# Kernel optimization log

Measured on AMD Instinct MI355X. Metric: run time of the kernel, lower is better.

Reference implementation:

```python
import jax, jax.numpy as jnp
import numpy as np

B, T, C = 2, 2048, 2048
H = 16
HD = C // H  # 128; kv_size == hidden_size so kv head dim == HD


def setup_inputs() -> dict:
    key = jax.random.key(0)
    ks = jax.random.split(key, 5)
    s = 0.02
    return {
        "x": jax.random.normal(ks[0], (B, T, C), dtype=jnp.float32),
        "Wq": jax.random.normal(ks[1], (C, C), dtype=jnp.float32) * s,
        "Wk": jax.random.normal(ks[2], (C, C), dtype=jnp.float32) * s,
        "Wv": jax.random.normal(ks[3], (C, C), dtype=jnp.float32) * s,
        "Wo": jax.random.normal(ks[4], (C, C), dtype=jnp.float32) * s,
    }


def reference(x, Wq, Wk, Wv, Wo):
    # Linear(bias=False): y = x @ W.T
    q = (x @ Wq.T).reshape(B, T, H, HD).transpose(0, 2, 1, 3)  # [B,H,T,HD]
    k = (x @ Wk.T).reshape(B, T, H, HD).transpose(0, 2, 1, 3)
    v = (x @ Wv.T).reshape(B, T, H, HD).transpose(0, 2, 1, 3)
    scale = 1.0 / np.sqrt(HD).astype(np.float32)
    att = jnp.einsum("bhqd,bhkd->bhqk", q, k) * scale  # [B,H,T,T]
    att = jax.nn.softmax(att, axis=-1)
    y = jnp.einsum("bhqk,bhkd->bhqd", att, v)  # [B,H,T,HD]
    y = y.transpose(0, 2, 1, 3).reshape(B, T, C)
    return y @ Wo.T
```

## Files before the change

kernel.cpp:

```cpp
#include <hip/hip_runtime.h>
#include <hip/hip_bf16.h>

typedef __attribute__((ext_vector_type(8))) short short8;
typedef __attribute__((ext_vector_type(4))) float f32x4;
typedef __attribute__((ext_vector_type(16))) float f32x16;
typedef unsigned short u16;
typedef unsigned int u32;

__device__ __forceinline__ u16 f2bf(float f){
  __hip_bfloat16 h = __float2bfloat16(f);
  return *reinterpret_cast<u16*>(&h);
}

__device__ __forceinline__ void gld16(const void* g, void* l){
  __builtin_amdgcn_global_load_lds((const __attribute__((address_space(1))) void*)g,
                                   (__attribute__((address_space(3))) void*)l, 16, 0, 0);
}

#define SCHED0() __builtin_amdgcn_sched_barrier(0)

__global__ __launch_bounds__(256) void cvt_kernel(const float* __restrict__ src,
                                                  u16* __restrict__ dst, int n){
  int i0 = (blockIdx.x*256 + threadIdx.x)*4;
  int stride = gridDim.x*256*4;
  for (int i = i0; i < n; i += stride){
    float4 f = *reinterpret_cast<const float4*>(src + i);
    ushort4 u;
    u.x = f2bf(f.x); u.y = f2bf(f.y); u.z = f2bf(f.z); u.w = f2bf(f.w);
    *reinterpret_cast<ushort4*>(dst + i) = u;
  }
}

__device__ __forceinline__ void gemm256_body(const u16* __restrict__ A,
    const u16* __restrict__ W, void* __restrict__ outp, float scale, int epi)
{
  __shared__ alignas(16) u16 Lds[2*24576];
  const int tid = threadIdx.x;
  const int w = tid>>6, l = tid&63;
  const int l15 = l&15, lg = l>>4;
  const int wm = w>>1, wn = w&1;
  const int row0 = blockIdx.y*256, col0 = blockIdx.x*128;
  constexpr int K = 2048;
  constexpr int NT = K/64;

  f32x4 acc[4][4];
  #pragma unroll
  for (int i=0;i<4;i++)
    #pragma unroll
    for (int j=0;j<4;j++)
      #pragma unroll
      for (int r=0;r<4;r++) acc[i][j][r] = 0.f;

  int arow[2], acol[2], brow[2], bcol[2];
  #pragma unroll
  for (int p=0;p<2;p++){
    int s = p*512 + tid;
    arow[p] = s>>2;  acol[p] = ((s&3) ^ (arow[p]&3))*8;
    brow[p] = s>>3;  bcol[p] = ((s&7) ^ (brow[p]&7))*8;
  }

  auto stageB = [&](int buf, int kt){
    #pragma unroll
    for (int p=0;p<2;p++)
      gld16(W + (size_t)(col0 + brow[p])*K + kt*64 + bcol[p],
            &Lds[buf*24576 + 16384 + (p*512 + w*64)*8]);
  };
  auto stageA = [&](int buf, int kt, int kh){
    #pragma unroll
    for (int p=0;p<2;p++)
      gld16(A + (size_t)(row0 + arow[p])*K + kt*64 + kh*32 + acol[p],
            &Lds[buf*24576 + kh*8192 + (p*512 + w*64)*8]);
  };
  auto readA = [&](int buf, int ks, short8* af){
    #pragma unroll
    for (int i=0;i<4;i++){
      int r = wm*64 + i*16 + l15;
      int byt = buf*49152 + ks*16384 + r*64 + ((lg ^ (r&3))<<4);
      af[i] = *reinterpret_cast<const short8*>((const char*)Lds + byt);
    }
  };
  auto readB = [&](int buf, int ks, short8* bf){
    #pragma unroll
    for (int j=0;j<4;j++){
      int r = wn*64 + j*16 + l15;
      int byt = buf*49152 + 32768 + r*128 + ((((ks<<2)|lg) ^ (r&7))<<4);
      bf[j] = *reinterpret_cast<const short8*>((const char*)Lds + byt);
    }
  };

  stageB(0, 0); stageA(0, 0, 0); stageA(0, 0, 1);
  SCHED0();
  asm volatile("s_waitcnt vmcnt(2)" ::: "memory");
  __builtin_amdgcn_s_barrier();
  SCHED0();

  int cur = 0;
  for (int t=0; t<NT; ++t){
    int nxt = (t+1) & (NT-1);
    int nbuf = cur^1;
    short8 af[4], bf[4];
    stageB(nbuf, nxt);
    stageA(nbuf, nxt, 0);
    readA(cur, 0, af); readB(cur, 0, bf);
    asm volatile("s_waitcnt lgkmcnt(0)" ::: "memory");
    SCHED0();
    __builtin_amdgcn_s_setprio(1);
    #pragma unroll
    for (int i=0;i<4;i++)
      #pragma unroll
      for (int j=0;j<4;j++)
        acc[i][j] = __builtin_amdgcn_mfma_f32_16x16x32_bf16(af[i], bf[j], acc[i][j], 0, 0, 0);
    __builtin_amdgcn_s_setprio(0);
    SCHED0();
    asm volatile("s_waitcnt vmcnt(4)" ::: "memory");
    __builtin_amdgcn_s_barrier();
    SCHED0();
    stageA(nbuf, nxt, 1);
    readA(cur, 1, af); readB(cur, 1, bf);
    asm volatile("s_waitcnt lgkmcnt(0)" ::: "memory");
    SCHED0();
    __builtin_amdgcn_s_setprio(1);
    #pragma unroll
    for (int i=0;i<4;i++)
      #pragma unroll
      for (int j=0;j<4;j++)
        acc[i][j] = __builtin_amdgcn_mfma_f32_16x16x32_bf16(af[i], bf[j], acc[i][j], 0, 0, 0);
    __builtin_amdgcn_s_setprio(0);
    SCHED0();
    asm volatile("s_waitcnt vmcnt(2)" ::: "memory");
    __builtin_amdgcn_s_barrier();
    SCHED0();
    cur ^= 1;
  }

  if (epi == 0){
    u16* O = (u16*)outp;
    #pragma unroll
    for (int i=0;i<4;i++)
      #pragma unroll
      for (int j=0;j<4;j++)
        #pragma unroll
        for (int r=0;r<4;r++){
          int m = row0 + wm*64 + i*16 + lg*4 + r;
          int n = col0 + wn*64 + j*16 + l15;
          int b = m >> 11, tt = m & 2047;
          int h = n >> 7,  d = n & 127;
          O[(((size_t)(b*16 + h)*2048 + tt)<<7) + d] = f2bf(acc[i][j][r] * scale);
        }
  } else if (epi == 2){
    u16* O = (u16*)outp;
    #pragma unroll
    for (int i=0;i<4;i++)
      #pragma unroll
      for (int j=0;j<4;j++){
        int m0 = row0 + wm*64 + i*16 + lg*4;
        int n  = col0 + wn*64 + j*16 + l15;
        int b = m0 >> 11, tt = m0 & 2047;
        int h = n >> 7,  d = n & 127;
        ushort4 u;
        u.x = f2bf(acc[i][j][0]); u.y = f2bf(acc[i][j][1]);
        u.z = f2bf(acc[i][j][2]); u.w = f2bf(acc[i][j][3]);
        *reinterpret_cast<ushort4*>(&O[(((size_t)(b*16 + h)<<7) + d)*2048 + tt]) = u;
      }
  } else {
    float* O = (float*)outp;
    #pragma unroll
    for (int i=0;i<4;i++)
      #pragma unroll
      for (int j=0;j<4;j++)
        #pragma unroll
        for (int r=0;r<4;r++){
          int m = row0 + wm*64 + i*16 + lg*4 + r;
          int n = col0 + wn*64 + j*16 + l15;
          O[(size_t)m*2048 + n] = acc[i][j][r];
        }
  }
}

__global__ __launch_bounds__(512,2) void gemm_qkv(const u16* __restrict__ A,
    const u16* __restrict__ Wq, const u16* __restrict__ Wk, const u16* __restrict__ Wv,
    u16* __restrict__ qo, u16* __restrict__ ko, u16* __restrict__ vt, float qscale)
{
  const u16* W; void* O; float sc; int epi;
  if (blockIdx.z == 0){ W = Wq; O = qo; sc = qscale; epi = 0; }
  else if (blockIdx.z == 1){ W = Wk; O = ko; sc = 1.f; epi = 0; }
  else { W = Wv; O = vt; sc = 1.f; epi = 2; }
  gemm256_body(A, W, O, sc, epi);
}

__global__ __launch_bounds__(512,2) void gemm_out(const u16* __restrict__ A,
    const u16* __restrict__ W, float* __restrict__ O)
{
  gemm256_body(A, W, O, 1.f, 1);
}

__global__ __launch_bounds__(256,2) void attn_kernel(
    const u16* __restrict__ Q, const u16* __restrict__ Kg,
    const u16* __restrict__ Vt, u16* __restrict__ Y)
{
  __shared__ alignas(16) u16 Ks[2][64*128];
  __shared__ alignas(16) u16 Vs[2][64*128];
  const int tid = threadIdx.x;
  const int w = tid>>6, l = tid&63;
  const int l31 = l&31, hi = l>>5;
  const int bh_swz = ((blockIdx.x&7)*64 + (blockIdx.x>>3));
  const int bh = bh_swz >> 4;
  const int q0 = (bh_swz & 15) * 128;

  short8 qf[8];
  #pragma unroll
  for (int ds=0; ds<8; ds++)
    qf[ds] = *reinterpret_cast<const short8*>(
        Q + ((size_t)bh*2048 + q0 + w*32 + l31)*128 + ds*16 + hi*8);

  f32x16 accO[4];
  #pragma unroll
  for (int dt=0;dt<4;dt++)
    #pragma unroll
    for (int r=0;r<16;r++) accO[dt][r] = 0.f;
  float mrun = -1e30f, lrun = 0.f;

  int krow_[4], kcol_[4], vd_[4], vkv_[4];
  #pragma unroll
  for (int p=0;p<4;p++){
    int s = p*256 + tid;
    int r = s>>4, c = s&15;
    int cu = c ^ (r&15);
    krow_[p] = r;  kcol_[p] = cu*8;
    vd_[p] = r*2 + (cu>>3);  vkv_[p] = (cu&7)*8;
  }

  auto stage = [&](int buf, int kvt){
    int kv0 = kvt*64;
    #pragma unroll
    for (int p=0;p<4;p++)
      gld16(Kg + ((size_t)bh*2048 + kv0 + krow_[p])*128 + kcol_[p],
            &Ks[buf][(size_t)(p*256 + w*64)*8]);
    #pragma unroll
    for (int p=0;p<4;p++)
      gld16(Vt + ((size_t)bh*128 + vd_[p])*2048 + kv0 + vkv_[p],
            &Vs[buf][(size_t)(p*256 + w*64)*8]);
  };

  stage(0, 0);
  __syncthreads();

  int cur = 0;
  for (int kvt=0; kvt<32; ++kvt){
    if (kvt+1 < 32) stage(cur^1, kvt+1);

    f32x16 accS[2];
    #pragma unroll
    for (int kt=0;kt<2;kt++)
      #pragma unroll
      for (int r=0;r<16;r++) accS[kt][r] = 0.f;
    #pragma unroll
    for (int kt=0;kt<2;kt++){
      #pragma unroll
      for (int ds=0;ds<8;ds++){
        int row = kt*32 + l31;
        int byt = row*256 + (((ds*2 + hi) ^ (row&15))<<4);
        short8 kf = *reinterpret_cast<const short8*>((const char*)(&Ks[cur][0]) + byt);
        accS[kt] = __builtin_amdgcn_mfma_f32_32x32x16_bf16(kf, qf[ds], accS[kt], 0, 0, 0);
      }
    }

    float pmax = accS[0][0];
    #pragma unroll
    for (int kt=0;kt<2;kt++)
      #pragma unroll
      for (int r=0;r<16;r++) pmax = fmaxf(pmax, accS[kt][r]);
    pmax = fmaxf(pmax, __shfl_xor(pmax, 32, 64));
    if (__any(pmax > mrun + 8.f)){
      float mn = fmaxf(mrun, pmax);
      float c = __expf(mrun - mn);
      mrun = mn;
      lrun *= c;
      #pragma unroll
      for (int r=0;r<16;r++){
        int qrow = (r&3) + 8*(r>>2) + 4*hi;
        float cr = __shfl(c, qrow, 64);
        #pragma unroll
        for (int dt=0;dt<4;dt++) accO[dt][r] *= cr;
      }
    }

    float rs = 0.f;
    short8 pa[4];
    #pragma unroll
    for (int kt=0;kt<2;kt++){
      #pragma unroll
      for (int b=0;b<2;b++){
        float e0 = __expf(accS[kt][b*8+0] - mrun);
        float e1 = __expf(accS[kt][b*8+1] - mrun);
        float e2 = __expf(accS[kt][b*8+2] - mrun);
        float e3 = __expf(accS[kt][b*8+3] - mrun);
        float e4 = __expf(accS[kt][b*8+4] - mrun);
        float e5 = __expf(accS[kt][b*8+5] - mrun);
        float e6 = __expf(accS[kt][b*8+6] - mrun);
        float e7 = __expf(accS[kt][b*8+7] - mrun);
        rs += (e0+e1)+(e2+e3)+(e4+e5)+(e6+e7);
        u32 x01 = (u32)f2bf(e0) | ((u32)f2bf(e1)<<16);
        u32 x23 = (u32)f2bf(e2) | ((u32)f2bf(e3)<<16);
        u32 y01 = (u32)f2bf(e4) | ((u32)f2bf(e5)<<16);
        u32 y23 = (u32)f2bf(e6) | ((u32)f2bf(e7)<<16);
        u32 sx_x01 = __shfl_xor(x01, 32, 64);
        u32 sx_x23 = __shfl_xor(x23, 32, 64);
        u32 sx_y01 = __shfl_xor(y01, 32, 64);
        u32 sx_y23 = __shfl_xor(y23, 32, 64);
        int4 wv;
        wv.x = (int)(hi ? sx_y01 : x01);
        wv.y = (int)(hi ? sx_y23 : x23);
        wv.z = (int)(hi ? y01 : sx_x01);
        wv.w = (int)(hi ? y23 : sx_x23);
        pa[kt*2+b] = *reinterpret_cast<short8*>(&wv);
      }
    }
    rs += __shfl_xor(rs, 32, 64);
    lrun += rs;

    #pragma unroll
    for (int dt=0;dt<4;dt++){
      #pragma unroll
      for (int ks=0;ks<4;ks++){
        int d = dt*32 + l31;
        int cu = (d&1)*8 + ks*2 + hi;
        int byt = (d>>1)*256 + ((cu ^ ((d>>1)&15))<<4);
        short8 vf = *reinterpret_cast<const short8*>((const char*)(&Vs[cur][0]) + byt);
        accO[dt] = __builtin_amdgcn_mfma_f32_32x32x16_bf16(pa[ks], vf, accO[dt], 0, 0, 0);
      }
    }

    __syncthreads();
    cur ^= 1;
  }

  const int b_ = bh >> 4, h_ = bh & 15;
  float inv = 1.f / lrun;
  #pragma unroll
  for (int r=0;r<16;r++){
    int qrow = (r&3) + 8*(r>>2) + 4*hi;
    float lr = __shfl(inv, qrow, 64);
    int t = q0 + w*32 + qrow;
    #pragma unroll
    for (int dt=0;dt<4;dt++){
      int d = dt*32 + l31;
      Y[((size_t)b_*2048 + t)*2048 + h_*128 + d] = f2bf(accO[dt][r] * lr);
    }
  }
}

extern "C" void kernel_launch(void* const* d_in, const int* in_sizes, int n_in,
                              void* d_out, int out_size, void* d_ws, size_t ws_size,
                              hipStream_t stream)
{
  const float* x  = (const float*)d_in[0];
  const float* Wq = (const float*)d_in[1];
  const float* Wk = (const float*)d_in[2];
  const float* Wv = (const float*)d_in[3];
  const float* Wo = (const float*)d_in[4];
  float* out = (float*)d_out;
  char* ws = (char*)d_ws;

  const size_t MB = 1024*1024;
  u16* xb  = (u16*)(ws);
  u16* wqb = (u16*)(ws + 16*MB);
  u16* wkb = (u16*)(ws + 24*MB);
  u16* wvb = (u16*)(ws + 32*MB);
  u16* wob = (u16*)(ws + 40*MB);
  u16* qb  = (u16*)(ws + 48*MB);
  u16* kb  = (u16*)(ws + 64*MB);
  u16* vtb = (u16*)(ws + 80*MB);
  u16* yb  = wqb;

  cvt_kernel<<<2048, 256, 0, stream>>>(x,  xb,  4096*2048);
  cvt_kernel<<<1024, 256, 0, stream>>>(Wq, wqb, 2048*2048);
  cvt_kernel<<<1024, 256, 0, stream>>>(Wk, wkb, 2048*2048);
  cvt_kernel<<<1024, 256, 0, stream>>>(Wv, wvb, 2048*2048);
  cvt_kernel<<<1024, 256, 0, stream>>>(Wo, wob, 2048*2048);

  const float qscale = 0.08838834764831845f;
  gemm_qkv<<<dim3(16,16,3), 512, 0, stream>>>(xb, wqb, wkb, wvb, qb, kb, vtb, qscale);
  attn_kernel<<<512, 256, 0, stream>>>(qb, kb, vtb, yb);
  gemm_out<<<dim3(16,16), 512, 0, stream>>>(yb, wob, out);
}
```

Before: 266.8 us.

## Restructure GEMM to 128x256 tiles with four-quadrant interleaved load/compute schedule

Changes the shared GEMM body from 256x128 to 128x256 block tiles. Each k-step is split into four quadrant MFMA groups, so loading the next tile's A and B halves interleaves with computing on quadrants of the current tile. Wave assignment moves to a 2x4 layout, and the LDS swizzle for A changes to 128-byte rows. The goal is better overlap of global-to-LDS copies with MFMA work, at the cost of more barriers per iteration and fiddly vmcnt accounting that could cause stalls or races.

```diff
diff --git a/kernel.cpp b/kernel.cpp
--- a/kernel.cpp
+++ b/kernel.cpp
@@ -34,12 +34,12 @@
 __device__ __forceinline__ void gemm256_body(const u16* __restrict__ A,
     const u16* __restrict__ W, void* __restrict__ outp, float scale, int epi)
 {
-  __shared__ alignas(16) u16 Lds[2*24576];
+  __shared__ alignas(16) u16 Lds[49152];
   const int tid = threadIdx.x;
   const int w = tid>>6, l = tid&63;
   const int l15 = l&15, lg = l>>4;
-  const int wm = w>>1, wn = w&1;
-  const int row0 = blockIdx.y*256, col0 = blockIdx.x*128;
+  const int wm = w&1, wn = w>>1;
+  const int row0 = blockIdx.y*128, col0 = blockIdx.x*256;
   constexpr int K = 2048;
   constexpr int NT = K/64;
 
@@ -51,83 +51,109 @@
       #pragma unroll
       for (int r=0;r<4;r++) acc[i][j][r] = 0.f;
 
-  int arow[2], acol[2], brow[2], bcol[2];
+  const int sArow = tid>>3,        sAcol = (((tid&7) ^ ((tid>>3)&7)))*8;
+  int sBrow[2], sBcol[2];
   #pragma unroll
   for (int p=0;p<2;p++){
     int s = p*512 + tid;
-    arow[p] = s>>2;  acol[p] = ((s&3) ^ (arow[p]&3))*8;
-    brow[p] = s>>3;  bcol[p] = ((s&7) ^ (brow[p]&7))*8;
-  }
-
-  auto stageB = [&](int buf, int kt){
+    sBrow[p] = s>>3;  sBcol[p] = ((s&7) ^ ((s>>3)&7))*8;
+  }
+
+  auto stageAh = [&](int slot, int kt, int h){
+    gld16(A + (size_t)(row0 + h*64 + sArow)*K + kt*64 + sAcol,
+          (char*)Lds + slot*49152 + h*8192 + w*1024);
+  };
+  auto stageBh = [&](int slot, int kt, int h){
     #pragma unroll
     for (int p=0;p<2;p++)
-      gld16(W + (size_t)(col0 + brow[p])*K + kt*64 + bcol[p],
-            &Lds[buf*24576 + 16384 + (p*512 + w*64)*8]);
-  };
-  auto stageA = [&](int buf, int kt, int kh){
-    #pragma unroll
-    for (int p=0;p<2;p++)
-      gld16(A + (size_t)(row0 + arow[p])*K + kt*64 + kh*32 + acol[p],
-            &Lds[buf*24576 + kh*8192 + (p*512 + w*64)*8]);
-  };
-  auto readA = [&](int buf, int ks, short8* af){
-    #pragma unroll
-    for (int i=0;i<4;i++){
-      int r = wm*64 + i*16 + l15;
-      int byt = buf*49152 + ks*16384 + r*64 + ((lg ^ (r&3))<<4);
-      af[i] = *reinterpret_cast<const short8*>((const char*)Lds + byt);
-    }
-  };
-  auto readB = [&](int buf, int ks, short8* bf){
-    #pragma unroll
-    for (int j=0;j<4;j++){
-      int r = wn*64 + j*16 + l15;
-      int byt = buf*49152 + 32768 + r*128 + ((((ks<<2)|lg) ^ (r&7))<<4);
-      bf[j] = *reinterpret_cast<const short8*>((const char*)Lds + byt);
-    }
-  };
-
-  stageB(0, 0); stageA(0, 0, 0); stageA(0, 0, 1);
-  SCHED0();
-  asm volatile("s_waitcnt vmcnt(2)" ::: "memory");
-  __builtin_amdgcn_s_barrier();
-  SCHED0();
+      gld16(W + (size_t)(col0 + h*128 + sBrow[p])*K + kt*64 + sBcol[p],
+            (char*)Lds + slot*49152 + 16384 + h*16384 + p*8192 + w*1024);
+  };
+  auto readA = [&](int slot, int mh, short8 (&af)[2][2]){
+    #pragma unroll
+    for (int ks=0;ks<2;ks++)
+      #pragma unroll
+      for (int i=0;i<2;i++){
+        int r = wm*32 + i*16 + l15;
+        int byt = slot*49152 + mh*8192 + r*128 + (((ks*4+lg) ^ (r&7))<<4);
+        af[ks][i] = *reinterpret_cast<const short8*>((const char*)Lds + byt);
+      }
+  };
+  auto readB = [&](int slot, int nh, short8 (&bf)[2][2]){
+    #pragma unroll
+    for (int ks=0;ks<2;ks++)
+      #pragma unroll
+      for (int j=0;j<2;j++){
+        int r = wn*32 + j*16 + l15;
+        int byt = slot*49152 + 16384 + nh*16384 + r*128 + (((ks*4+lg) ^ (r&7))<<4);
+        bf[ks][j] = *reinterpret_cast<const short8*>((const char*)Lds + byt);
+      }
+  };
+
+  short8 a0[2][2], a1[2][2], bb[2][2];
+  auto quad = [&](const short8 (&af)[2][2], int mh, int nh){
+    #pragma unroll
+    for (int ks=0;ks<2;ks++)
+      #pragma unroll
+      for (int i=0;i<2;i++)
+        #pragma unroll
+        for (int j=0;j<2;j++)
+          acc[mh*2+i][nh*2+j] = __builtin_amdgcn_mfma_f32_16x16x32_bf16(
+              af[ks][i], bb[ks][j], acc[mh*2+i][nh*2+j], 0, 0, 0);
+  };
+
+  stageAh(0,0,0); stageBh(0,0,0); stageAh(0,0,1); stageBh(0,0,1);
+  __syncthreads();
 
   int cur = 0;
   for (int t=0; t<NT; ++t){
     int nxt = (t+1) & (NT-1);
-    int nbuf = cur^1;
-    short8 af[4], bf[4];
-    stageB(nbuf, nxt);
-    stageA(nbuf, nxt, 0);
-    readA(cur, 0, af); readB(cur, 0, bf);
+    int ns = cur^1;
+    readA(cur, 0, a0);
+    readB(cur, 0, bb);
+    stageAh(ns, nxt, 0);
+    stageBh(ns, nxt, 0);
+    SCHED0();
+    __builtin_amdgcn_s_barrier();
     asm volatile("s_waitcnt lgkmcnt(0)" ::: "memory");
     SCHED0();
     __builtin_amdgcn_s_setprio(1);
-    #pragma unroll
-    for (int i=0;i<4;i++)
-      #pragma unroll
-      for (int j=0;j<4;j++)
-        acc[i][j] = __builtin_amdgcn_mfma_f32_16x16x32_bf16(af[i], bf[j], acc[i][j], 0, 0, 0);
+    quad(a0, 0, 0);
     __builtin_amdgcn_s_setprio(0);
     SCHED0();
+    asm volatile("s_waitcnt vmcnt(5)" ::: "memory");
+    __builtin_amdgcn_s_barrier();
+    SCHED0();
+    readA(cur, 1, a1);
+    stageAh(ns, nxt, 1);
+    SCHED0();
+    __builtin_amdgcn_s_barrier();
+    asm volatile("s_waitcnt lgkmcnt(0)" ::: "memory");
+    SCHED0();
+    __builtin_amdgcn_s_setprio(1);
+    quad(a1, 1, 0);
+    __builtin_amdgcn_s_setprio(0);
+    SCHED0();
     asm volatile("s_waitcnt vmcnt(4)" ::: "memory");
     __builtin_amdgcn_s_barrier();
     SCHED0();
-    stageA(nbuf, nxt, 1);
-    readA(cur, 1, af); readB(cur, 1, bf);
+    readB(cur, 1, bb);
+    stageBh(ns, nxt, 1);
+    SCHED0();
+    __builtin_amdgcn_s_barrier();
     asm volatile("s_waitcnt lgkmcnt(0)" ::: "memory");
     SCHED0();
     __builtin_amdgcn_s_setprio(1);
-    #pragma unroll
-    for (int i=0;i<4;i++)
-      #pragma unroll
-      for (int j=0;j<4;j++)
-        acc[i][j] = __builtin_amdgcn_mfma_f32_16x16x32_bf16(af[i], bf[j], acc[i][j], 0, 0, 0);
+    quad(a1, 1, 1);
     __builtin_amdgcn_s_setprio(0);
     SCHED0();
-    asm volatile("s_waitcnt vmcnt(2)" ::: "memory");
+    __builtin_amdgcn_s_barrier();
+    SCHED0();
+    __builtin_amdgcn_s_setprio(1);
+    quad(a0, 0, 1);
+    __builtin_amdgcn_s_setprio(0);
+    SCHED0();
+    asm volatile("s_waitcnt vmcnt(3)" ::: "memory");
     __builtin_amdgcn_s_barrier();
     SCHED0();
     cur ^= 1;
@@ -136,43 +162,43 @@
   if (epi == 0){
     u16* O = (u16*)outp;
     #pragma unroll
-    for (int i=0;i<4;i++)
-      #pragma unroll
-      for (int j=0;j<4;j++)
+    for (int mi=0;mi<4;mi++)
+      #pragma unroll
+      for (int nj=0;nj<4;nj++)
         #pragma unroll
         for (int r=0;r<4;r++){
-          int m = row0 + wm*64 + i*16 + lg*4 + r;
-          int n = col0 + wn*64 + j*16 + l15;
+          int m = row0 + (mi>>1)*64 + wm*32 + (mi&1)*16 + lg*4 + r;
+          int n = col0 + (nj>>1)*128 + wn*32 + (nj&1)*16 + l15;
           int b = m >> 11, tt = m & 2047;
           int h = n >> 7,  d = n & 127;
-          O[(((size_t)(b*16 + h)*2048 + tt)<<7) + d] = f2bf(acc[i][j][r] * scale);
+          O[(((size_t)(b*16 + h)*2048 + tt)<<7) + d] = f2bf(acc[mi][nj][r] * scale);
         }
   } else if (epi == 2){
     u16* O = (u16*)outp;
     #pragma unroll
-    for (int i=0;i<4;i++)
-      #pragma unroll
-      for (int j=0;j<4;j++){
-        int m0 = row0 + wm*64 + i*16 + lg*4;
-        int n  = col0 + wn*64 + j*16 + l15;
+    for (int mi=0;mi<4;mi++)
+      #pragma unroll
+      for (int nj=0;nj<4;nj++){
+        int m0 = row0 + (mi>>1)*64 + wm*32 + (mi&1)*16 + lg*4;
+        int n  = col0 + (nj>>1)*128 + wn*32 + (nj&1)*16 + l15;
         int b = m0 >> 11, tt = m0 & 2047;
         int h = n >> 7,  d = n & 127;
         ushort4 u;
-        u.x = f2bf(acc[i][j][0]); u.y = f2bf(acc[i][j][1]);
-        u.z = f2bf(acc[i][j][2]); u.w = f2bf(acc[i][j][3]);
+        u.x = f2bf(acc[mi][nj][0]); u.y = f2bf(acc[mi][nj][1]);
+        u.z = f2bf(acc[mi][nj][2]); u.w = f2bf(acc[mi][nj][3]);
         *reinterpret_cast<ushort4*>(&O[(((size_t)(b*16 + h)<<7) + d)*2048 + tt]) = u;
       }
   } else {
     float* O = (float*)outp;
     #pragma unroll
-    for (int i=0;i<4;i++)
-      #pragma unroll
-      for (int j=0;j<4;j++)
+    for (int mi=0;mi<4;mi++)
+      #pragma unroll
+      for (int nj=0;nj<4;nj++)
         #pragma unroll
         for (int r=0;r<4;r++){
-          int m = row0 + wm*64 + i*16 + lg*4 + r;
-          int n = col0 + wn*64 + j*16 + l15;
-          O[(size_t)m*2048 + n] = acc[i][j][r];
+          int m = row0 + (mi>>1)*64 + wm*32 + (mi&1)*16 + lg*4 + r;
+          int n = col0 + (nj>>1)*128 + wn*32 + (nj&1)*16 + l15;
+          O[(size_t)m*2048 + n] = acc[mi][nj][r];
         }
   }
 }
@@ -380,7 +406,7 @@
   cvt_kernel<<<1024, 256, 0, stream>>>(Wo, wob, 2048*2048);
 
   const float qscale = 0.08838834764831845f;
-  gemm_qkv<<<dim3(16,16,3), 512, 0, stream>>>(xb, wqb, wkb, wvb, qb, kb, vtb, qscale);
+  gemm_qkv<<<dim3(8,32,3), 512, 0, stream>>>(xb, wqb, wkb, wvb, qb, kb, vtb, qscale);
   attn_kernel<<<512, 256, 0, stream>>>(qb, kb, vtb, yb);
-  gemm_out<<<dim3(16,16), 512, 0, stream>>>(yb, wob, out);
-}
+  gemm_out<<<dim3(8,32), 512, 0, stream>>>(yb, wob, out);
+}
```

Result: no change. 263.6 us (-1.2%).

## Restructure GEMM to 128x256 tiles with split-K waves and triple buffering

Applied to the files above, without the earlier changes.

The shared GEMM body changes from 256x128 tiles to 128x256 tiles. The 8 waves are split into two K-halves (wk) that each handle half of every 64-wide K slice and are reduced through LDS at the end. The LDS ring grows from double to triple buffering with a prefetch distance of two tiles, and there is one barrier per K tile instead of two. The aim is better latency hiding and fewer barriers per tile. In exchange, LDS use rises to 144KB per block, which may drop occupancy to one block per CU, and the split-K reduction adds an epilogue cost.

```diff
diff --git a/kernel.cpp b/kernel.cpp
--- a/kernel.cpp
+++ b/kernel.cpp
@@ -34,146 +34,156 @@
 __device__ __forceinline__ void gemm256_body(const u16* __restrict__ A,
     const u16* __restrict__ W, void* __restrict__ outp, float scale, int epi)
 {
-  __shared__ alignas(16) u16 Lds[2*24576];
+  __shared__ alignas(16) u16 Lds[73728];
   const int tid = threadIdx.x;
   const int w = tid>>6, l = tid&63;
   const int l15 = l&15, lg = l>>4;
-  const int wm = w>>1, wn = w&1;
-  const int row0 = blockIdx.y*256, col0 = blockIdx.x*128;
+  const int wm = w&1, wn = (w>>1)&1, wk = w>>2;
+  const int row0 = blockIdx.y*128, col0 = blockIdx.x*256;
   constexpr int K = 2048;
   constexpr int NT = K/64;
 
-  f32x4 acc[4][4];
+  f32x4 acc[4][8];
   #pragma unroll
   for (int i=0;i<4;i++)
     #pragma unroll
-    for (int j=0;j<4;j++)
+    for (int j=0;j<8;j++)
       #pragma unroll
       for (int r=0;r<4;r++) acc[i][j][r] = 0.f;
 
-  int arow[2], acol[2], brow[2], bcol[2];
-  #pragma unroll
-  for (int p=0;p<2;p++){
+  int sBrow[4], sBcol[4];
+  #pragma unroll
+  for (int p=0;p<4;p++){
     int s = p*512 + tid;
-    arow[p] = s>>2;  acol[p] = ((s&3) ^ (arow[p]&3))*8;
-    brow[p] = s>>3;  bcol[p] = ((s&7) ^ (brow[p]&7))*8;
-  }
-
-  auto stageB = [&](int buf, int kt){
-    #pragma unroll
-    for (int p=0;p<2;p++)
-      gld16(W + (size_t)(col0 + brow[p])*K + kt*64 + bcol[p],
-            &Lds[buf*24576 + 16384 + (p*512 + w*64)*8]);
-  };
-  auto stageA = [&](int buf, int kt, int kh){
-    #pragma unroll
-    for (int p=0;p<2;p++)
-      gld16(A + (size_t)(row0 + arow[p])*K + kt*64 + kh*32 + acol[p],
-            &Lds[buf*24576 + kh*8192 + (p*512 + w*64)*8]);
-  };
-  auto readA = [&](int buf, int ks, short8* af){
+    sBrow[p] = s>>3;  sBcol[p] = ((s&7) ^ ((s>>3)&7))*8;
+  }
+  const int sArow0 = sBrow[0], sAcol0 = sBcol[0];
+  const int sArow1 = sBrow[1], sAcol1 = sBcol[1];
+
+  auto stageA = [&](int slot, int kt){
+    gld16(A + (size_t)(row0 + sArow0)*K + kt*64 + sAcol0,
+          &Lds[slot*8192 + (size_t)(w*64)*8]);
+    gld16(A + (size_t)(row0 + sArow1)*K + kt*64 + sAcol1,
+          &Lds[slot*8192 + (size_t)(512 + w*64)*8]);
+  };
+  auto stageB = [&](int slot, int kt){
+    #pragma unroll
+    for (int p=0;p<4;p++)
+      gld16(W + (size_t)(col0 + sBrow[p])*K + kt*64 + sBcol[p],
+            &Lds[24576 + slot*16384 + (size_t)(p*512 + w*64)*8]);
+  };
+  auto readA = [&](int slot, short8 (&af)[4]){
     #pragma unroll
     for (int i=0;i<4;i++){
       int r = wm*64 + i*16 + l15;
-      int byt = buf*49152 + ks*16384 + r*64 + ((lg ^ (r&3))<<4);
+      int byt = slot*16384 + r*128 + (((wk*4+lg) ^ (r&7))<<4);
       af[i] = *reinterpret_cast<const short8*>((const char*)Lds + byt);
     }
   };
-  auto readB = [&](int buf, int ks, short8* bf){
-    #pragma unroll
-    for (int j=0;j<4;j++){
-      int r = wn*64 + j*16 + l15;
-      int byt = buf*49152 + 32768 + r*128 + ((((ks<<2)|lg) ^ (r&7))<<4);
+  auto readB = [&](int slot, short8 (&bf)[8]){
+    #pragma unroll
+    for (int j=0;j<8;j++){
+      int r = wn*128 + j*16 + l15;
+      int byt = 49152 + slot*32768 + r*128 + (((wk*4+lg) ^ (r&7))<<4);
       bf[j] = *reinterpret_cast<const short8*>((const char*)Lds + byt);
     }
   };
 
-  stageB(0, 0); stageA(0, 0, 0); stageA(0, 0, 1);
+  stageA(0, 0); stageB(0, 0);
+  stageA(1, 1); stageB(1, 1);
   SCHED0();
-  asm volatile("s_waitcnt vmcnt(2)" ::: "memory");
+  asm volatile("s_waitcnt vmcnt(6)" ::: "memory");
   __builtin_amdgcn_s_barrier();
   SCHED0();
 
-  int cur = 0;
+  int sl = 0;
   for (int t=0; t<NT; ++t){
-    int nxt = (t+1) & (NT-1);
-    int nbuf = cur^1;
-    short8 af[4], bf[4];
-    stageB(nbuf, nxt);
-    stageA(nbuf, nxt, 0);
-    readA(cur, 0, af); readB(cur, 0, bf);
+    int st = sl+2; if (st>=3) st-=3;
+    int tn = (t+2) & (NT-1);
+    stageA(st, tn);
+    stageB(st, tn);
+    short8 af[4], bf[8];
+    readA(sl, af);
+    readB(sl, bf);
     asm volatile("s_waitcnt lgkmcnt(0)" ::: "memory");
     SCHED0();
     __builtin_amdgcn_s_setprio(1);
     #pragma unroll
     for (int i=0;i<4;i++)
       #pragma unroll
-      for (int j=0;j<4;j++)
+      for (int j=0;j<8;j++)
         acc[i][j] = __builtin_amdgcn_mfma_f32_16x16x32_bf16(af[i], bf[j], acc[i][j], 0, 0, 0);
     __builtin_amdgcn_s_setprio(0);
     SCHED0();
-    asm volatile("s_waitcnt vmcnt(4)" ::: "memory");
+    asm volatile("s_waitcnt vmcnt(6)" ::: "memory");
     __builtin_amdgcn_s_barrier();
     SCHED0();
-    stageA(nbuf, nxt, 1);
-    readA(cur, 1, af); readB(cur, 1, bf);
-    asm volatile("s_waitcnt lgkmcnt(0)" ::: "memory");
-    SCHED0();
-    __builtin_amdgcn_s_setprio(1);
+    sl = sl+1; if (sl>=3) sl = 0;
+  }
+
+  __syncthreads();
+  float* R = (float*)Lds;
+  const int pair = wm*2 + wn;
+  if (wk == 1){
     #pragma unroll
     for (int i=0;i<4;i++)
       #pragma unroll
-      for (int j=0;j<4;j++)
-        acc[i][j] = __builtin_amdgcn_mfma_f32_16x16x32_bf16(af[i], bf[j], acc[i][j], 0, 0, 0);
-    __builtin_amdgcn_s_setprio(0);
-    SCHED0();
-    asm volatile("s_waitcnt vmcnt(2)" ::: "memory");
-    __builtin_amdgcn_s_barrier();
-    SCHED0();
-    cur ^= 1;
-  }
-
-  if (epi == 0){
-    u16* O = (u16*)outp;
+      for (int j=0;j<8;j++)
+        *reinterpret_cast<f32x4*>(&R[pair*8192 + (i*8+j)*256 + l*4]) = acc[i][j];
+  }
+  __syncthreads();
+  if (wk == 0){
     #pragma unroll
     for (int i=0;i<4;i++)
       #pragma unroll
-      for (int j=0;j<4;j++)
-        #pragma unroll
-        for (int r=0;r<4;r++){
-          int m = row0 + wm*64 + i*16 + lg*4 + r;
-          int n = col0 + wn*64 + j*16 + l15;
-          int b = m >> 11, tt = m & 2047;
+      for (int j=0;j<8;j++){
+        f32x4 o = *reinterpret_cast<const f32x4*>(&R[pair*8192 + (i*8+j)*256 + l*4]);
+        #pragma unroll
+        for (int r=0;r<4;r++) acc[i][j][r] += o[r];
+      }
+
+    if (epi == 0){
+      u16* O = (u16*)outp;
+      #pragma unroll
+      for (int i=0;i<4;i++)
+        #pragma unroll
+        for (int j=0;j<8;j++)
+          #pragma unroll
+          for (int r=0;r<4;r++){
+            int m = row0 + wm*64 + i*16 + lg*4 + r;
+            int n = col0 + wn*128 + j*16 + l15;
+            int b = m >> 11, tt = m & 2047;
+            int h = n >> 7,  d = n & 127;
+            O[(((size_t)(b*16 + h)*2048 + tt)<<7) + d] = f2bf(acc[i][j][r] * scale);
+          }
+    } else if (epi == 2){
+      u16* O = (u16*)outp;
+      #pragma unroll
+      for (int i=0;i<4;i++)
+        #pragma unroll
+        for (int j=0;j<8;j++){
+          int m0 = row0 + wm*64 + i*16 + lg*4;
+          int n  = col0 + wn*128 + j*16 + l15;
+          int b = m0 >> 11, tt = m0 & 2047;
           int h = n >> 7,  d = n & 127;
-          O[(((size_t)(b*16 + h)*2048 + tt)<<7) + d] = f2bf(acc[i][j][r] * scale);
+          ushort4 u;
+          u.x = f2bf(acc[i][j][0]); u.y = f2bf(acc[i][j][1]);
+          u.z = f2bf(acc[i][j][2]); u.w = f2bf(acc[i][j][3]);
+          *reinterpret_cast<ushort4*>(&O[(((size_t)(b*16 + h)<<7) + d)*2048 + tt]) = u;
         }
-  } else if (epi == 2){
-    u16* O = (u16*)outp;
-    #pragma unroll
-    for (int i=0;i<4;i++)
-      #pragma unroll
-      for (int j=0;j<4;j++){
-        int m0 = row0 + wm*64 + i*16 + lg*4;
-        int n  = col0 + wn*64 + j*16 + l15;
-        int b = m0 >> 11, tt = m0 & 2047;
-        int h = n >> 7,  d = n & 127;
-        ushort4 u;
-        u.x = f2bf(acc[i][j][0]); u.y = f2bf(acc[i][j][1]);
-        u.z = f2bf(acc[i][j][2]); u.w = f2bf(acc[i][j][3]);
-        *reinterpret_cast<ushort4*>(&O[(((size_t)(b*16 + h)<<7) + d)*2048 + tt]) = u;
-      }
-  } else {
-    float* O = (float*)outp;
-    #pragma unroll
-    for (int i=0;i<4;i++)
-      #pragma unroll
-      for (int j=0;j<4;j++)
-        #pragma unroll
-        for (int r=0;r<4;r++){
-          int m = row0 + wm*64 + i*16 + lg*4 + r;
-          int n = col0 + wn*64 + j*16 + l15;
-          O[(size_t)m*2048 + n] = acc[i][j][r];
-        }
+    } else {
+      float* O = (float*)outp;
+      #pragma unroll
+      for (int i=0;i<4;i++)
+        #pragma unroll
+        for (int j=0;j<8;j++)
+          #pragma unroll
+          for (int r=0;r<4;r++){
+            int m = row0 + wm*64 + i*16 + lg*4 + r;
+            int n = col0 + wn*128 + j*16 + l15;
+            O[(size_t)m*2048 + n] = acc[i][j][r];
+          }
+    }
   }
 }
 
@@ -380,7 +390,7 @@
   cvt_kernel<<<1024, 256, 0, stream>>>(Wo, wob, 2048*2048);
 
   const float qscale = 0.08838834764831845f;
-  gemm_qkv<<<dim3(16,16,3), 512, 0, stream>>>(xb, wqb, wkb, wvb, qb, kb, vtb, qscale);
+  gemm_qkv<<<dim3(8,32,3), 512, 0, stream>>>(xb, wqb, wkb, wvb, qb, kb, vtb, qscale);
   attn_kernel<<<512, 256, 0, stream>>>(qb, kb, vtb, yb);
-  gemm_out<<<dim3(16,16), 512, 0, stream>>>(yb, wob, out);
-}
+  gemm_out<<<dim3(8,32), 512, 0, stream>>>(yb, wob, out);
+}
```

New measurement: 263.6 us. About the same (-1.2%).
